# Kernel tuning notes

Measured on AMD Instinct MI355X. Metric: run time of the kernel, lower is better.

## Reference

```python
import jax, jax.numpy as jnp
from jax import lax
import numpy as np

B, H, W = 16, 512, 512
OPENING_R, EROSION_R, DILATION_R = 5, 2, 1
MIN_SIZE, AREA_THRESHOLD = 2000, 300
INF = np.int32(2 ** 30)


def _disk(r):
    # skimage.morphology.disk: x^2 + y^2 <= r^2 on a (2r+1)^2 grid
    y, x = np.mgrid[-r:r + 1, -r:r + 1]
    return jnp.asarray((x * x + y * y <= r * r).astype(np.float32))


D_OPEN, D_ERODE, D_DILATE = _disk(OPENING_R), _disk(EROSION_R), _disk(DILATION_R)


def _conv2(x, k):
    return lax.conv_general_dilated(x[None, None], k[None, None], (1, 1), 'VALID')[0, 0]


def _erode(fg, se):
    # skimage binary_erosion uses border_value=True (image border does not erode)
    r = se.shape[0] // 2
    x = jnp.pad(fg.astype(jnp.float32), r, constant_values=1.0)
    return _conv2(x, se) >= se.sum() - 0.5


def _dilate(fg, se):
    # skimage binary_dilation uses border_value=False
    r = se.shape[0] // 2
    x = jnp.pad(fg.astype(jnp.float32), r, constant_values=0.0)
    return _conv2(x, se) > 0.5


def _seg_cummin(v, reset, axis, reverse):
    # segmented cumulative-min: scan resets wherever `reset` is True (background)
    def comb(a, b):
        av, af = a
        bv, bf = b
        return jnp.where(bf, bv, jnp.minimum(av, bv)), af | bf

    vv, _ = lax.associative_scan(comb, (v, reset), axis=axis, reverse=reverse)
    return vv


def _label(fg):
    # 4-connectivity connected-component labeling via min-label propagation.
    # Each fg pixel starts with its raveled index; alternating row/col segmented
    # cummin sweeps run under while_loop until a fixed point (root id per comp).
    h, w = fg.shape
    idx = jnp.arange(h * w, dtype=jnp.int32).reshape(h, w)
    lab0 = jnp.where(fg, idx, INF)
    bg = ~fg

    def sweep(l):
        for axis in (1, 0):
            for rev in (False, True):
                l = jnp.where(fg, _seg_cummin(l, bg, axis, rev), INF)
        return l

    def body(c):
        l, _ = c
        nl = sweep(l)
        return nl, jnp.array_equal(nl, l)

    lab, _ = lax.while_loop(lambda c: ~c[1], body, (lab0, jnp.array(False)))
    seg = jnp.where(fg, lab, 0).ravel()
    sizes = jax.ops.segment_sum(fg.astype(jnp.int32).ravel(), seg, num_segments=h * w)
    ncomp = jnp.sum(sizes > 0)
    return lab, sizes, ncomp


def _remove_small_objects(fg, min_size, guard):
    lab, sizes, ncomp = _label(fg)
    px = sizes[jnp.where(fg, lab, 0)]  # component size at every fg pixel
    kept = fg & (px >= min_size)
    # original only removes small objects when label(...).max() > 1
    return jnp.where(ncomp > 1, kept, fg) if guard else kept


def _pipeline(mask):
    fg = mask > 0
    fg = _remove_small_objects(fg, MIN_SIZE, True)
    # remove_small_holes == ~remove_small_objects(~fg, area_threshold + 1)
    fg = ~_remove_small_objects(~fg, AREA_THRESHOLD + 1, False)
    fg = _erode(fg, D_ERODE)
    fg = _dilate(_erode(fg, D_OPEN), D_OPEN)  # binary_opening
    fg = _remove_small_objects(fg, MIN_SIZE, True)
    fg = _dilate(fg, D_DILATE)
    return fg.astype(jnp.float32)  # original casts to int; float32 kept for vjp parity


def setup_inputs() -> dict:
    key = jax.random.key(0)
    # blobby binary masks: threshold bilinearly-upsampled low-res noise so that
    # realistic large connected components (> min_size px) exist
    low = jax.random.uniform(key, (B, H // 16, W // 16), dtype=jnp.float32)
    blob = jax.image.resize(low, (B, H, W), method='bilinear')
    return {'inputs': (blob > 0.5).astype(jnp.float32)}


def reference(inputs):
    return jax.vmap(_pipeline)(inputs)
```

## Files before the change

kernel.cpp:

```cpp
#include <hip/hip_runtime.h>
#include <stdint.h>

#define BATCH 16
#define H 512
#define W 512
#define HW (H * W)
#define NTOT (BATCH * HW)
#define NWORDS (NTOT / 64)

#define TPB 256
#define NBLK ((NTOT + TPB - 1) / TPB)
#define NBLKW ((NWORDS + TPB - 1) / TPB)

#define SROWS 16
#define SWORDS 128
#define SPIX 8192
#define NSTRIPS (NWORDS / SWORDS)

__device__ __forceinline__ int find_root_c(int* L, int x) {
    int r = x, p = L[r];
    while (p != r) { r = p; p = L[r]; }
    if (L[x] != r) atomicMin(&L[x], r);
    return r;
}

__device__ void merge_uf(int* L, int a, int b) {
    while (true) {
        a = find_root_c(L, a);
        b = find_root_c(L, b);
        if (a == b) return;
        int lo = a < b ? a : b;
        int hi = a < b ? b : a;
        int old = atomicMin(&L[hi], lo);
        if (old == hi) return;
        a = lo; b = old;
    }
}

__device__ __forceinline__ int find_root_lds(int* P, int x) {
    int r = x, p = P[r];
    while (p != r) { r = p; p = P[r]; }
    return r;
}

__device__ void merge_lds(int* P, int a, int b) {
    while (true) {
        a = find_root_lds(P, a);
        b = find_root_lds(P, b);
        if (a == b) return;
        int lo = a < b ? a : b;
        int hi = a < b ? b : a;
        int old = atomicMin(&P[hi], lo);
        if (old == hi) return;
        a = lo; b = old;
    }
}

__device__ __forceinline__ int start_of(uint64_t m, int i, int cv, int base) {
    uint64_t below = i ? ((~m) & ((1ull << i) - 1)) : 0ull;
    if (below == 0) return (cv >= 0) ? cv : base;
    int hz = 63 - __builtin_clzll(below);
    return base + hz + 1;
}

__device__ uint64_t keep_word(const uint64_t* __restrict__ bits,
                              const int* __restrict__ carry, const int* __restrict__ L,
                              const int* __restrict__ sizes, const int* __restrict__ ncomp,
                              int minsz, int gw) {
    uint64_t m = bits[gw];
    uint64_t res = m;
    if (m && ncomp[gw >> 12] > 1) {
        int cv = carry[gw];
        int base = gw << 6;
        while (m) {
            int s = __builtin_ctzll(m);
            uint64_t rest = m >> s;
            uint64_t nr = ~rest;
            int len = nr ? __builtin_ctzll(nr) : (64 - s);
            uint64_t piece = ((len >= 64) ? ~0ull : ((1ull << len) - 1)) << s;
            int start = (s == 0 && cv >= 0) ? cv : (base + s);
            if (sizes[L[start]] < minsz) res &= ~piece;
            m &= ~piece;
        }
    }
    return res;
}

__device__ uint64_t fill_word(const uint64_t* __restrict__ bits,
                              const int* __restrict__ carry, const int* __restrict__ L,
                              const int* __restrict__ sizes, int minsz, int gw) {
    uint64_t fg = bits[gw];
    uint64_t bg = ~fg;
    uint64_t res = fg;
    int cv = carry[gw];
    int base = gw << 6;
    while (bg) {
        int s = __builtin_ctzll(bg);
        uint64_t rest = bg >> s;
        uint64_t nr = ~rest;
        int len = nr ? __builtin_ctzll(nr) : (64 - s);
        uint64_t piece = ((len >= 64) ? ~0ull : ((1ull << len) - 1)) << s;
        int start = (s == 0 && cv >= 0) ? cv : (base + s);
        if (sizes[L[start]] < minsz) res |= piece;
        bg &= ~piece;
    }
    return res;
}

template <int R, bool ERODE>
__device__ uint64_t morph_word_lds(const uint64_t* buf, int lrow, int w, int gyTop) {
    const uint64_t BORDER = ERODE ? ~0ull : 0ull;
    uint64_t res = ERODE ? ~0ull : 0ull;
#pragma unroll
    for (int dy = -R; dy <= R; ++dy) {
        int lr = lrow + dy;
        int gy = gyTop + lr;
        if (gy < 0 || gy >= H) continue;
        int v = R * R - dy * dy;
        int kx = 0;
        while ((kx + 1) * (kx + 1) <= v) ++kx;
        uint64_t cur = buf[lr * 8 + w];
        uint64_t prv = (w > 0) ? buf[lr * 8 + w - 1] : BORDER;
        uint64_t nxt = (w < 7) ? buf[lr * 8 + w + 1] : BORDER;
        uint64_t acc = cur;
#pragma unroll
        for (int dx = 1; dx <= kx; ++dx) {
            uint64_t right = (cur >> dx) | (nxt << (64 - dx));
            uint64_t left  = (cur << dx) | (prv >> (64 - dx));
            if (ERODE) acc &= right & left;
            else       acc |= right | left;
        }
        if (ERODE) res &= acc;
        else       res |= acc;
    }
    return res;
}

__device__ void strip_ccl_body(uint64_t m, uint64_t* sw, int* scarry, int* par,
                               int blk, int t,
                               int* __restrict__ carry, int* __restrict__ L,
                               int* __restrict__ sizes, int* __restrict__ ncomp) {
    sw[t] = m;
    __syncthreads();

    if (t < SROWS) {
        int cv = -1;
        for (int i = 0; i < 8; ++i) {
            int lw = t * 8 + i;
            scarry[lw] = cv;
            uint64_t w = sw[lw];
            if (w >> 63) {
                uint64_t z = ~w;
                if (z == 0) { if (cv < 0) cv = lw << 6; }
                else { int hz = 63 - __builtin_clzll(z); cv = (lw << 6) + hz + 1; }
            } else cv = -1;
        }
    }
    __syncthreads();

    int cv = scarry[t];
    carry[blk * SWORDS + t] = (cv >= 0) ? (blk * SPIX + cv) : -1;
    int lbase = t << 6;
    uint64_t starts = m & ~((m << 1) | ((cv >= 0) ? 1ull : 0ull));
    uint64_t ss = starts;
    while (ss) {
        int s = __builtin_ctzll(ss);
        par[lbase + s] = lbase + s;
        ss &= ss - 1;
    }
    __syncthreads();

    if (t >= 8 && m) {
        uint64_t up = sw[t - 8];
        uint64_t cand = m & up;
        if (cand) {
            uint64_t curprev = (t & 7) ? sw[t - 1] : 0ull;
            uint64_t upprev  = (t & 7) ? sw[t - 9] : 0ull;
            uint64_t curl = (m << 1) | (curprev >> 63);
            uint64_t upl  = (up << 1) | (upprev >> 63);
            cand &= ~(curl & upl);
            int cvu = scarry[t - 8];
            while (cand) {
                int i = __builtin_ctzll(cand);
                int sP = start_of(m, i, cv, lbase);
                int sQ = start_of(up, i, cvu, lbase - 512);
                merge_lds(par, sP, sQ);
                cand &= cand - 1;
            }
        }
    }
    __syncthreads();

    int gpix = blk * SPIX;
    ss = starts;
    while (ss) {
        int s = __builtin_ctzll(ss);
        int ls = lbase + s;
        int r = find_root_lds(par, ls);
        L[gpix + ls] = gpix + r;
        if (r == ls) sizes[gpix + ls] = 0;
        ss &= ss - 1;
    }
    if (t == 0 && (blk & 31) == 0) ncomp[blk >> 5] = 0;
}

__global__ void k_thresh_pack(const float* __restrict__ in, uint64_t* __restrict__ bits) {
    int p = blockIdx.x * blockDim.x + threadIdx.x;
    bool a = (p < NTOT) && (in[p] > 0.0f);
    uint64_t b = __ballot(a);
    if ((threadIdx.x & 63) == 0 && p < NTOT) bits[p >> 6] = b;
}

__global__ void k_strip_ccl(const uint64_t* __restrict__ bits, int inv,
                            int* __restrict__ carry, int* __restrict__ L,
                            int* __restrict__ sizes, int* __restrict__ ncomp) {
    __shared__ uint64_t sw[SWORDS];
    __shared__ int scarry[SWORDS];
    __shared__ int par[SPIX];
    int blk = blockIdx.x;
    int t = threadIdx.x;
    uint64_t inv64 = inv ? ~0ull : 0ull;
    uint64_t m = bits[blk * SWORDS + t] ^ inv64;
    strip_ccl_body(m, sw, scarry, par, blk, t, carry, L, sizes, ncomp);
}

__global__ void k_keep_strip(const uint64_t* __restrict__ bits,
                             const int* __restrict__ carryIn, const int* __restrict__ Lin,
                             const int* __restrict__ sizesIn, const int* __restrict__ ncompIn,
                             uint64_t* __restrict__ outBits,
                             int* __restrict__ carryOut, int* __restrict__ Lout,
                             int* __restrict__ sizesOut, int* __restrict__ ncompOut) {
    __shared__ uint64_t sw[SWORDS];
    __shared__ int scarry[SWORDS];
    __shared__ int par[SPIX];
    int blk = blockIdx.x;
    int t = threadIdx.x;
    int gw = blk * SWORDS + t;
    uint64_t kw = keep_word(bits, carryIn, Lin, sizesIn, ncompIn, 2000, gw);
    outBits[gw] = kw;
    strip_ccl_body(~kw, sw, scarry, par, blk, t, carryOut, Lout, sizesOut, ncompOut);
}

__global__ void k_merge_bound(const uint64_t* __restrict__ bits, int inv,
                              const int* __restrict__ carry, int* __restrict__ L) {
    int tid = threadIdx.x;
    if (tid >= 248) return;
    int img = blockIdx.x;
    int y = ((tid >> 3) + 1) * SROWS;
    int w = tid & 7;
    int gw = img * 4096 + y * 8 + w;
    uint64_t inv64 = inv ? ~0ull : 0ull;
    uint64_t cur = bits[gw] ^ inv64;
    uint64_t up  = bits[gw - 8] ^ inv64;
    uint64_t cand = cur & up;
    if (!cand) return;
    uint64_t curprev = w ? (bits[gw - 1] ^ inv64) : 0ull;
    uint64_t upprev  = w ? (bits[gw - 9] ^ inv64) : 0ull;
    uint64_t curl = (cur << 1) | (curprev >> 63);
    uint64_t upl  = (up << 1)  | (upprev >> 63);
    cand &= ~(curl & upl);
    if (!cand) return;
    int cvc = carry[gw], cvu = carry[gw - 8];
    int base = gw << 6;
    while (cand) {
        int i = __builtin_ctzll(cand);
        int sP = start_of(cur, i, cvc, base);
        int sQ = start_of(up, i, cvu, base - W);
        merge_uf(L, sP, sQ);
        cand &= cand - 1;
    }
}

__global__ void k_flatten_count(const uint64_t* __restrict__ bits, int inv,
                                const int* __restrict__ carry, int* __restrict__ L,
                                int* __restrict__ sizes, int* __restrict__ ncomp) {
    __shared__ int hk[128];
    __shared__ int hv[128];
    for (int i = threadIdx.x; i < 128; i += TPB) { hk[i] = -1; hv[i] = 0; }
    __syncthreads();

    int gw = blockIdx.x * blockDim.x + threadIdx.x;
    if (gw < NWORDS) {
        uint64_t inv64 = inv ? ~0ull : 0ull;
        uint64_t m = bits[gw] ^ inv64;
        if (m) {
            int cv = carry[gw];
            int base = gw << 6;
            while (m) {
                int s = __builtin_ctzll(m);
                uint64_t rest = m >> s;
                uint64_t nr = ~rest;
                int len = nr ? __builtin_ctzll(nr) : (64 - s);
                uint64_t piece = ((len >= 64) ? ~0ull : ((1ull << len) - 1)) << s;
                bool initial = !(s == 0 && cv >= 0);
                int start = initial ? (base + s) : cv;
                int r = find_root_c(L, start);
                if (initial && r == start) atomicAdd(&ncomp[gw >> 12], 1);
                int cnt = __popcll(piece);
                uint32_t h = ((uint32_t)r * 2654435761u) >> 25;
                bool done = false;
                for (int tt = 0; tt < 16; ++tt) {
                    int slot = (h + tt) & 127;
                    int k = hk[slot];
                    if (k == -1) k = atomicCAS(&hk[slot], -1, r);
                    if (k == -1 || k == r) { atomicAdd(&hv[slot], cnt); done = true; break; }
                }
                if (!done) atomicAdd(&sizes[r], cnt);
                m &= ~piece;
            }
        }
    }
    __syncthreads();
    for (int i = threadIdx.x; i < 128; i += TPB)
        if (hk[i] != -1) atomicAdd(&sizes[hk[i]], hv[i]);
}

__global__ void k_fill_morph(const uint64_t* __restrict__ bits,
                             const int* __restrict__ carry, const int* __restrict__ L,
                             const int* __restrict__ sizes,
                             uint64_t* __restrict__ out) {
    __shared__ uint64_t bufA[56 * 8];
    __shared__ uint64_t bufB[56 * 8];
    int img = blockIdx.x >> 4;
    int s   = blockIdx.x & 15;
    int y0 = s * 32;
    int gyTop = y0 - 12;
    int t = threadIdx.x;

    for (int lw = t; lw < 56 * 8; lw += TPB) {
        int gy = gyTop + (lw >> 3);
        int w = lw & 7;
        uint64_t v = 0;
        if (gy >= 0 && gy < H)
            v = fill_word(bits, carry, L, sizes, 301, img * 4096 + gy * 8 + w);
        bufA[lw] = v;
    }
    __syncthreads();

    for (int lw = t; lw < 56 * 8; lw += TPB) {
        int lr = lw >> 3;
        if (lr < 2 || lr > 53) continue;
        bufB[lw] = morph_word_lds<2, true>(bufA, lr, lw & 7, gyTop);
    }
    __syncthreads();

    for (int lw = t; lw < 56 * 8; lw += TPB) {
        int lr = lw >> 3;
        if (lr < 7 || lr > 48) continue;
        bufA[lw] = morph_word_lds<5, true>(bufB, lr, lw & 7, gyTop);
    }
    __syncthreads();

    for (int lw = t; lw < 56 * 8; lw += TPB) {
        int lr = lw >> 3;
        if (lr < 12 || lr > 43) continue;
        uint64_t v = morph_word_lds<5, false>(bufA, lr, lw & 7, gyTop);
        int gy = gyTop + lr;
        out[img * 4096 + gy * 8 + (lw & 7)] = v;
    }
}

__global__ void k_keep_dilate_float(const uint64_t* __restrict__ bits,
                                    const int* __restrict__ carry, const int* __restrict__ L,
                                    const int* __restrict__ sizes, const int* __restrict__ ncomp,
                                    float* __restrict__ out) {
    __shared__ uint64_t kb[10 * 8];
    __shared__ uint64_t db[8 * 8];
    int blk = blockIdx.x;
    int img = blk >> 6;
    int s = blk & 63;
    int y0 = s * 8;
    int t = threadIdx.x;

    if (t < 80) {
        int lr = t >> 3;
        int w = t & 7;
        int gy = y0 - 1 + lr;
        uint64_t v = 0;
        if (gy >= 0 && gy < H)
            v = keep_word(bits, carry, L, sizes, ncomp, 2000, img * 4096 + gy * 8 + w);
        kb[t] = v;
    }
    __syncthreads();
    if (t < 64) {
        int r = t >> 3, w = t & 7;
        uint64_t cur = kb[(r + 1) * 8 + w];
        uint64_t up  = kb[r * 8 + w];
        uint64_t dn  = kb[(r + 2) * 8 + w];
        uint64_t prv = w ? kb[(r + 1) * 8 + w - 1] : 0ull;
        uint64_t nxt = (w < 7) ? kb[(r + 1) * 8 + w + 1] : 0ull;
        db[t] = cur | up | dn | (cur << 1) | (prv >> 63) | (cur >> 1) | (nxt << 63);
    }
    __syncthreads();

    int q0 = t * 16;
    uint64_t wd = db[q0 >> 6];
    int sh = q0 & 63;
    float4* o = (float4*)(out + (size_t)img * HW + (size_t)y0 * W + q0);
#pragma unroll
    for (int k = 0; k < 4; ++k) {
        uint32_t nib = (uint32_t)(wd >> (sh + k * 4)) & 0xFu;
        float4 f;
        f.x = (nib & 1u) ? 1.0f : 0.0f;
        f.y = (nib & 2u) ? 1.0f : 0.0f;
        f.z = (nib & 4u) ? 1.0f : 0.0f;
        f.w = (nib & 8u) ? 1.0f : 0.0f;
        o[k] = f;
    }
}

extern "C" void kernel_launch(void* const* d_in, const int* in_sizes, int n_in,
                              void* d_out, int out_size, void* d_ws, size_t ws_size,
                              hipStream_t stream) {
    const float* in = (const float*)d_in[0];
    float* out = (float*)d_out;

    uint8_t* ws = (uint8_t*)d_ws;
    int* LA      = (int*)ws;
    int* sizesA  = (int*)(ws + (size_t)NTOT * 4);
    int* LB      = (int*)(ws + (size_t)NTOT * 8);
    int* sizesB  = (int*)(ws + (size_t)NTOT * 12);
    uint64_t* bitsA = (uint64_t*)(ws + (size_t)NTOT * 16);
    uint64_t* bitsB = bitsA + NWORDS;
    uint64_t* bits3 = bitsB + NWORDS;
    int* carryA = (int*)(bits3 + NWORDS);
    int* carryB = carryA + NWORDS;
    int* ncompA = carryB + NWORDS;
    int* ncompB = ncompA + BATCH;

    k_thresh_pack<<<NBLK, TPB, 0, stream>>>(in, bitsA);

    k_strip_ccl<<<NSTRIPS, SWORDS, 0, stream>>>(bitsA, 0, carryA, LA, sizesA, ncompA);
    k_merge_bound<<<BATCH, 256, 0, stream>>>(bitsA, 0, carryA, LA);
    k_flatten_count<<<NBLKW, TPB, 0, stream>>>(bitsA, 0, carryA, LA, sizesA, ncompA);

    k_keep_strip<<<NSTRIPS, SWORDS, 0, stream>>>(bitsA, carryA, LA, sizesA, ncompA,
                                                 bitsB, carryB, LB, sizesB, ncompB);
    k_merge_bound<<<BATCH, 256, 0, stream>>>(bitsB, 1, carryB, LB);
    k_flatten_count<<<NBLKW, TPB, 0, stream>>>(bitsB, 1, carryB, LB, sizesB, ncompB);

    k_fill_morph<<<BATCH * 16, TPB, 0, stream>>>(bitsB, carryB, LB, sizesB, bits3);

    k_strip_ccl<<<NSTRIPS, SWORDS, 0, stream>>>(bits3, 0, carryA, LA, sizesA, ncompA);
    k_merge_bound<<<BATCH, 256, 0, stream>>>(bits3, 0, carryA, LA);
    k_flatten_count<<<NBLKW, TPB, 0, stream>>>(bits3, 0, carryA, LA, sizesA, ncompA);

    k_keep_dilate_float<<<BATCH * 64, TPB, 0, stream>>>(bits3, carryA, LA, sizesA, ncompA, out);
}
```

Baseline: 204.0 us.

## Fuse CCL, fill and morphology stages into one cooperative persistent kernel

Replaces the sequence of nine launches (strip CCL, boundary merge, flatten/count for three labeling passes plus fill+morph) with a single cooperative kernel. Stages are separated by grid.sync, and the fill+morphology step is re-tiled to 16-row strips matching the CCL strip so it feeds the next labeling directly from LDS. The goal is to cut launch gaps and inter-kernel drain, at the cost of grid-wide barriers, 128-thread blocks and more redundant halo work in the morphology stage.

```diff
diff --git a/kernel.cpp b/kernel.cpp
--- a/kernel.cpp
+++ b/kernel.cpp
@@ -1,5 +1,8 @@
 #include <hip/hip_runtime.h>
+#include <hip/hip_cooperative_groups.h>
 #include <stdint.h>
+
+namespace cg = cooperative_groups;
 
 #define BATCH 16
 #define H 512
@@ -10,7 +13,6 @@
 
 #define TPB 256
 #define NBLK ((NTOT + TPB - 1) / TPB)
-#define NBLKW ((NWORDS + TPB - 1) / TPB)
 
 #define SROWS 16
 #define SWORDS 128
@@ -204,50 +206,14 @@
     if (t == 0 && (blk & 31) == 0) ncomp[blk >> 5] = 0;
 }
 
-__global__ void k_thresh_pack(const float* __restrict__ in, uint64_t* __restrict__ bits) {
-    int p = blockIdx.x * blockDim.x + threadIdx.x;
-    bool a = (p < NTOT) && (in[p] > 0.0f);
-    uint64_t b = __ballot(a);
-    if ((threadIdx.x & 63) == 0 && p < NTOT) bits[p >> 6] = b;
-}
-
-__global__ void k_strip_ccl(const uint64_t* __restrict__ bits, int inv,
-                            int* __restrict__ carry, int* __restrict__ L,
-                            int* __restrict__ sizes, int* __restrict__ ncomp) {
-    __shared__ uint64_t sw[SWORDS];
-    __shared__ int scarry[SWORDS];
-    __shared__ int par[SPIX];
-    int blk = blockIdx.x;
-    int t = threadIdx.x;
-    uint64_t inv64 = inv ? ~0ull : 0ull;
-    uint64_t m = bits[blk * SWORDS + t] ^ inv64;
-    strip_ccl_body(m, sw, scarry, par, blk, t, carry, L, sizes, ncomp);
-}
-
-__global__ void k_keep_strip(const uint64_t* __restrict__ bits,
-                             const int* __restrict__ carryIn, const int* __restrict__ Lin,
-                             const int* __restrict__ sizesIn, const int* __restrict__ ncompIn,
-                             uint64_t* __restrict__ outBits,
-                             int* __restrict__ carryOut, int* __restrict__ Lout,
-                             int* __restrict__ sizesOut, int* __restrict__ ncompOut) {
-    __shared__ uint64_t sw[SWORDS];
-    __shared__ int scarry[SWORDS];
-    __shared__ int par[SPIX];
-    int blk = blockIdx.x;
-    int t = threadIdx.x;
-    int gw = blk * SWORDS + t;
-    uint64_t kw = keep_word(bits, carryIn, Lin, sizesIn, ncompIn, 2000, gw);
-    outBits[gw] = kw;
-    strip_ccl_body(~kw, sw, scarry, par, blk, t, carryOut, Lout, sizesOut, ncompOut);
-}
-
-__global__ void k_merge_bound(const uint64_t* __restrict__ bits, int inv,
-                              const int* __restrict__ carry, int* __restrict__ L) {
-    int tid = threadIdx.x;
-    if (tid >= 248) return;
-    int img = blockIdx.x;
-    int y = ((tid >> 3) + 1) * SROWS;
-    int w = tid & 7;
+__device__ void merge_bound_dev(const uint64_t* __restrict__ bits, int inv,
+                                const int* __restrict__ carry, int* __restrict__ L,
+                                int flat) {
+    if (flat >= BATCH * 31 * 8) return;
+    int img = flat / 248;
+    int rem = flat - img * 248;
+    int y = ((rem >> 3) + 1) * SROWS;
+    int w = rem & 7;
     int gw = img * 4096 + y * 8 + w;
     uint64_t inv64 = inv ? ~0ull : 0ull;
     uint64_t cur = bits[gw] ^ inv64;
@@ -271,93 +237,125 @@
     }
 }
 
-__global__ void k_flatten_count(const uint64_t* __restrict__ bits, int inv,
-                                const int* __restrict__ carry, int* __restrict__ L,
-                                int* __restrict__ sizes, int* __restrict__ ncomp) {
+__device__ void flatten_count_dev(const uint64_t* __restrict__ bits, int inv,
+                                  const int* __restrict__ carry, int* __restrict__ L,
+                                  int* __restrict__ sizes, int* __restrict__ ncomp,
+                                  int gw, int t, int* hk, int* hv) {
+    hk[t] = -1; hv[t] = 0;
+    __syncthreads();
+    uint64_t inv64 = inv ? ~0ull : 0ull;
+    uint64_t m = bits[gw] ^ inv64;
+    if (m) {
+        int cv = carry[gw];
+        int base = gw << 6;
+        while (m) {
+            int s = __builtin_ctzll(m);
+            uint64_t rest = m >> s;
+            uint64_t nr = ~rest;
+            int len = nr ? __builtin_ctzll(nr) : (64 - s);
+            uint64_t piece = ((len >= 64) ? ~0ull : ((1ull << len) - 1)) << s;
+            bool initial = !(s == 0 && cv >= 0);
+            int start = initial ? (base + s) : cv;
+            int r = find_root_c(L, start);
+            if (initial && r == start) atomicAdd(&ncomp[gw >> 12], 1);
+            int cnt = __popcll(piece);
+            uint32_t h = ((uint32_t)r * 2654435761u) >> 25;
+            bool done = false;
+            for (int tt = 0; tt < 16; ++tt) {
+                int slot = (h + tt) & 127;
+                int k = hk[slot];
+                if (k == -1) k = atomicCAS(&hk[slot], -1, r);
+                if (k == -1 || k == r) { atomicAdd(&hv[slot], cnt); done = true; break; }
+            }
+            if (!done) atomicAdd(&sizes[r], cnt);
+            m &= ~piece;
+        }
+    }
+    __syncthreads();
+    if (hk[t] != -1) atomicAdd(&sizes[hk[t]], hv[t]);
+    __syncthreads();
+}
+
+__global__ void k_thresh_pack(const float* __restrict__ in, uint64_t* __restrict__ bits) {
+    int p = blockIdx.x * blockDim.x + threadIdx.x;
+    bool a = (p < NTOT) && (in[p] > 0.0f);
+    uint64_t b = __ballot(a);
+    if ((threadIdx.x & 63) == 0 && p < NTOT) bits[p >> 6] = b;
+}
+
+__global__ __launch_bounds__(SWORDS, 2)
+void k_mega(const uint64_t* __restrict__ bits1, uint64_t* __restrict__ bits2,
+            uint64_t* __restrict__ bits3,
+            int* __restrict__ carryA, int* __restrict__ carryB,
+            int* __restrict__ LA, int* __restrict__ LB,
+            int* __restrict__ sizesA, int* __restrict__ sizesB,
+            int* __restrict__ ncompA, int* __restrict__ ncompB) {
+    cg::grid_group grid = cg::this_grid();
+    __shared__ uint64_t sw[SWORDS];
+    __shared__ int scarry[SWORDS];
     __shared__ int hk[128];
     __shared__ int hv[128];
-    for (int i = threadIdx.x; i < 128; i += TPB) { hk[i] = -1; hv[i] = 0; }
-    __syncthreads();
-
-    int gw = blockIdx.x * blockDim.x + threadIdx.x;
-    if (gw < NWORDS) {
-        uint64_t inv64 = inv ? ~0ull : 0ull;
-        uint64_t m = bits[gw] ^ inv64;
-        if (m) {
-            int cv = carry[gw];
-            int base = gw << 6;
-            while (m) {
-                int s = __builtin_ctzll(m);
-                uint64_t rest = m >> s;
-                uint64_t nr = ~rest;
-                int len = nr ? __builtin_ctzll(nr) : (64 - s);
-                uint64_t piece = ((len >= 64) ? ~0ull : ((1ull << len) - 1)) << s;
-                bool initial = !(s == 0 && cv >= 0);
-                int start = initial ? (base + s) : cv;
-                int r = find_root_c(L, start);
-                if (initial && r == start) atomicAdd(&ncomp[gw >> 12], 1);
-                int cnt = __popcll(piece);
-                uint32_t h = ((uint32_t)r * 2654435761u) >> 25;
-                bool done = false;
-                for (int tt = 0; tt < 16; ++tt) {
-                    int slot = (h + tt) & 127;
-                    int k = hk[slot];
-                    if (k == -1) k = atomicCAS(&hk[slot], -1, r);
-                    if (k == -1 || k == r) { atomicAdd(&hv[slot], cnt); done = true; break; }
-                }
-                if (!done) atomicAdd(&sizes[r], cnt);
-                m &= ~piece;
-            }
-        }
-    }
-    __syncthreads();
-    for (int i = threadIdx.x; i < 128; i += TPB)
-        if (hk[i] != -1) atomicAdd(&sizes[hk[i]], hv[i]);
-}
-
-__global__ void k_fill_morph(const uint64_t* __restrict__ bits,
-                             const int* __restrict__ carry, const int* __restrict__ L,
-                             const int* __restrict__ sizes,
-                             uint64_t* __restrict__ out) {
-    __shared__ uint64_t bufA[56 * 8];
-    __shared__ uint64_t bufB[56 * 8];
-    int img = blockIdx.x >> 4;
-    int s   = blockIdx.x & 15;
-    int y0 = s * 32;
-    int gyTop = y0 - 12;
+    __shared__ union {
+        int par[SPIX];
+        struct { uint64_t A[320]; uint64_t B[320]; } mo;
+    } U;
+    int s = blockIdx.x;
     int t = threadIdx.x;
-
-    for (int lw = t; lw < 56 * 8; lw += TPB) {
-        int gy = gyTop + (lw >> 3);
-        int w = lw & 7;
-        uint64_t v = 0;
-        if (gy >= 0 && gy < H)
-            v = fill_word(bits, carry, L, sizes, 301, img * 4096 + gy * 8 + w);
-        bufA[lw] = v;
-    }
-    __syncthreads();
-
-    for (int lw = t; lw < 56 * 8; lw += TPB) {
-        int lr = lw >> 3;
-        if (lr < 2 || lr > 53) continue;
-        bufB[lw] = morph_word_lds<2, true>(bufA, lr, lw & 7, gyTop);
-    }
-    __syncthreads();
-
-    for (int lw = t; lw < 56 * 8; lw += TPB) {
-        int lr = lw >> 3;
-        if (lr < 7 || lr > 48) continue;
-        bufA[lw] = morph_word_lds<5, true>(bufB, lr, lw & 7, gyTop);
-    }
-    __syncthreads();
-
-    for (int lw = t; lw < 56 * 8; lw += TPB) {
-        int lr = lw >> 3;
-        if (lr < 12 || lr > 43) continue;
-        uint64_t v = morph_word_lds<5, false>(bufA, lr, lw & 7, gyTop);
-        int gy = gyTop + lr;
-        out[img * 4096 + gy * 8 + (lw & 7)] = v;
-    }
+    int gw = s * SWORDS + t;
+    int flat = s * SWORDS + t;
+
+    strip_ccl_body(bits1[gw], sw, scarry, U.par, s, t, carryA, LA, sizesA, ncompA);
+    grid.sync();
+    merge_bound_dev(bits1, 0, carryA, LA, flat);
+    grid.sync();
+    flatten_count_dev(bits1, 0, carryA, LA, sizesA, ncompA, gw, t, hk, hv);
+    grid.sync();
+
+    uint64_t kw = keep_word(bits1, carryA, LA, sizesA, ncompA, 2000, gw);
+    bits2[gw] = kw;
+    strip_ccl_body(~kw, sw, scarry, U.par, s, t, carryB, LB, sizesB, ncompB);
+    grid.sync();
+    merge_bound_dev(bits2, 1, carryB, LB, flat);
+    grid.sync();
+    flatten_count_dev(bits2, 1, carryB, LB, sizesB, ncompB, gw, t, hk, hv);
+    grid.sync();
+
+    uint64_t m3;
+    {
+        int img = s >> 5, si = s & 31;
+        int gyTop = si * 16 - 12;
+        for (int lw = t; lw < 320; lw += SWORDS) {
+            int gy = gyTop + (lw >> 3);
+            int w = lw & 7;
+            uint64_t v = 0;
+            if (gy >= 0 && gy < H)
+                v = fill_word(bits2, carryB, LB, sizesB, 301, img * 4096 + gy * 8 + w);
+            U.mo.A[lw] = v;
+        }
+        __syncthreads();
+        for (int lw = t; lw < 320; lw += SWORDS) {
+            int lr = lw >> 3;
+            if (lr >= 2 && lr <= 37) U.mo.B[lw] = morph_word_lds<2, true>(U.mo.A, lr, lw & 7, gyTop);
+        }
+        __syncthreads();
+        for (int lw = t; lw < 320; lw += SWORDS) {
+            int lr = lw >> 3;
+            if (lr >= 7 && lr <= 32) U.mo.A[lw] = morph_word_lds<5, true>(U.mo.B, lr, lw & 7, gyTop);
+        }
+        __syncthreads();
+        for (int lw = t; lw < 320; lw += SWORDS) {
+            int lr = lw >> 3;
+            if (lr >= 12 && lr <= 27) U.mo.B[lw] = morph_word_lds<5, false>(U.mo.A, lr, lw & 7, gyTop);
+        }
+        __syncthreads();
+        m3 = U.mo.B[t + 96];
+        bits3[gw] = m3;
+    }
+    strip_ccl_body(m3, sw, scarry, U.par, s, t, carryA, LA, sizesA, ncompA);
+    grid.sync();
+    merge_bound_dev(bits3, 0, carryA, LA, flat);
+    grid.sync();
+    flatten_count_dev(bits3, 0, carryA, LA, sizesA, ncompA, gw, t, hk, hv);
 }
 
 __global__ void k_keep_dilate_float(const uint64_t* __restrict__ bits,
@@ -420,30 +418,21 @@
     int* sizesA  = (int*)(ws + (size_t)NTOT * 4);
     int* LB      = (int*)(ws + (size_t)NTOT * 8);
     int* sizesB  = (int*)(ws + (size_t)NTOT * 12);
-    uint64_t* bitsA = (uint64_t*)(ws + (size_t)NTOT * 16);
-    uint64_t* bitsB = bitsA + NWORDS;
-    uint64_t* bits3 = bitsB + NWORDS;
+    uint64_t* bits1 = (uint64_t*)(ws + (size_t)NTOT * 16);
+    uint64_t* bits2 = bits1 + NWORDS;
+    uint64_t* bits3 = bits2 + NWORDS;
     int* carryA = (int*)(bits3 + NWORDS);
     int* carryB = carryA + NWORDS;
     int* ncompA = carryB + NWORDS;
     int* ncompB = ncompA + BATCH;
 
-    k_thresh_pack<<<NBLK, TPB, 0, stream>>>(in, bitsA);
-
-    k_strip_ccl<<<NSTRIPS, SWORDS, 0, stream>>>(bitsA, 0, carryA, LA, sizesA, ncompA);
-    k_merge_bound<<<BATCH, 256, 0, stream>>>(bitsA, 0, carryA, LA);
-    k_flatten_count<<<NBLKW, TPB, 0, stream>>>(bitsA, 0, carryA, LA, sizesA, ncompA);
-
-    k_keep_strip<<<NSTRIPS, SWORDS, 0, stream>>>(bitsA, carryA, LA, sizesA, ncompA,
-                                                 bitsB, carryB, LB, sizesB, ncompB);
-    k_merge_bound<<<BATCH, 256, 0, stream>>>(bitsB, 1, carryB, LB);
-    k_flatten_count<<<NBLKW, TPB, 0, stream>>>(bitsB, 1, carryB, LB, sizesB, ncompB);
-
-    k_fill_morph<<<BATCH * 16, TPB, 0, stream>>>(bitsB, carryB, LB, sizesB, bits3);
-
-    k_strip_ccl<<<NSTRIPS, SWORDS, 0, stream>>>(bits3, 0, carryA, LA, sizesA, ncompA);
-    k_merge_bound<<<BATCH, 256, 0, stream>>>(bits3, 0, carryA, LA);
-    k_flatten_count<<<NBLKW, TPB, 0, stream>>>(bits3, 0, carryA, LA, sizesA, ncompA);
+    k_thresh_pack<<<NBLK, TPB, 0, stream>>>(in, bits1);
+
+    void* args[] = { (void*)&bits1, (void*)&bits2, (void*)&bits3,
+                     (void*)&carryA, (void*)&carryB, (void*)&LA, (void*)&LB,
+                     (void*)&sizesA, (void*)&sizesB, (void*)&ncompA, (void*)&ncompB };
+    hipLaunchCooperativeKernel((void*)k_mega, dim3(NSTRIPS), dim3(SWORDS),
+                               args, 0, stream);
 
     k_keep_dilate_float<<<BATCH * 64, TPB, 0, stream>>>(bits3, carryA, LA, sizesA, ncompA, out);
 }
```

After: 621.3 us. 205% more time.

## Fuse hole-fill and morphology into strip CCL kernel; vectorize threshold packing

Applied to the files above, without the earlier changes.

Merges the fill+erode+open stage with the following per-strip connected-component labeling into one kernel. Each 16-row strip recomputes its morphology over a 12-row halo in LDS (a union with the CCL parent array) and then labels the result directly, which removes a launch and a global round trip of the intermediate mask. The cost is more halo recomputation per output row, since strips shrink from 32 rows to 16. The threshold-pack kernel also now reads float4 and combines nibbles with shuffles.

```diff
diff --git a/kernel.cpp b/kernel.cpp
--- a/kernel.cpp
+++ b/kernel.cpp
@@ -9,7 +9,6 @@
 #define NWORDS (NTOT / 64)
 
 #define TPB 256
-#define NBLK ((NTOT + TPB - 1) / TPB)
 #define NBLKW ((NWORDS + TPB - 1) / TPB)
 
 #define SROWS 16
@@ -204,11 +203,20 @@
     if (t == 0 && (blk & 31) == 0) ncomp[blk >> 5] = 0;
 }
 
-__global__ void k_thresh_pack(const float* __restrict__ in, uint64_t* __restrict__ bits) {
-    int p = blockIdx.x * blockDim.x + threadIdx.x;
-    bool a = (p < NTOT) && (in[p] > 0.0f);
-    uint64_t b = __ballot(a);
-    if ((threadIdx.x & 63) == 0 && p < NTOT) bits[p >> 6] = b;
+
+__global__ void k_thresh_pack4(const float4* __restrict__ in4,
+                               uint64_t* __restrict__ bits) {
+    int q = blockIdx.x * blockDim.x + threadIdx.x;
+    if (q >= NTOT / 4) return;
+    float4 v = in4[q];
+    uint32_t nib = (v.x > 0.0f ? 1u : 0u) | (v.y > 0.0f ? 2u : 0u) |
+                   (v.z > 0.0f ? 4u : 0u) | (v.w > 0.0f ? 8u : 0u);
+    uint64_t val = (uint64_t)nib << (4 * (threadIdx.x & 15));
+    val |= __shfl_xor(val, 1);
+    val |= __shfl_xor(val, 2);
+    val |= __shfl_xor(val, 4);
+    val |= __shfl_xor(val, 8);
+    if ((threadIdx.x & 15) == 0) bits[q >> 4] = val;
 }
 
 __global__ void k_strip_ccl(const uint64_t* __restrict__ bits, int inv,
@@ -315,49 +323,50 @@
         if (hk[i] != -1) atomicAdd(&sizes[hk[i]], hv[i]);
 }
 
-__global__ void k_fill_morph(const uint64_t* __restrict__ bits,
-                             const int* __restrict__ carry, const int* __restrict__ L,
-                             const int* __restrict__ sizes,
-                             uint64_t* __restrict__ out) {
-    __shared__ uint64_t bufA[56 * 8];
-    __shared__ uint64_t bufB[56 * 8];
-    int img = blockIdx.x >> 4;
-    int s   = blockIdx.x & 15;
-    int y0 = s * 32;
-    int gyTop = y0 - 12;
+__global__ void k_fill_morph_ccl(const uint64_t* __restrict__ bits,
+                                 const int* __restrict__ carryB, const int* __restrict__ LB,
+                                 const int* __restrict__ sizesB,
+                                 uint64_t* __restrict__ bits3,
+                                 int* __restrict__ carryA, int* __restrict__ LA,
+                                 int* __restrict__ sizesA, int* __restrict__ ncompA) {
+    __shared__ uint64_t sw[SWORDS];
+    __shared__ int scarry[SWORDS];
+    __shared__ union {
+        int par[SPIX];
+        struct { uint64_t A[320]; uint64_t B[320]; } mo;
+    } U;
+    int s = blockIdx.x;
     int t = threadIdx.x;
-
-    for (int lw = t; lw < 56 * 8; lw += TPB) {
+    int img = s >> 5, si = s & 31;
+    int gyTop = si * 16 - 12;
+
+    for (int lw = t; lw < 320; lw += SWORDS) {
         int gy = gyTop + (lw >> 3);
         int w = lw & 7;
         uint64_t v = 0;
         if (gy >= 0 && gy < H)
-            v = fill_word(bits, carry, L, sizes, 301, img * 4096 + gy * 8 + w);
-        bufA[lw] = v;
-    }
-    __syncthreads();
-
-    for (int lw = t; lw < 56 * 8; lw += TPB) {
+            v = fill_word(bits, carryB, LB, sizesB, 301, img * 4096 + gy * 8 + w);
+        U.mo.A[lw] = v;
+    }
+    __syncthreads();
+    for (int lw = t; lw < 320; lw += SWORDS) {
         int lr = lw >> 3;
-        if (lr < 2 || lr > 53) continue;
-        bufB[lw] = morph_word_lds<2, true>(bufA, lr, lw & 7, gyTop);
-    }
-    __syncthreads();
-
-    for (int lw = t; lw < 56 * 8; lw += TPB) {
+        if (lr >= 2 && lr <= 37) U.mo.B[lw] = morph_word_lds<2, true>(U.mo.A, lr, lw & 7, gyTop);
+    }
+    __syncthreads();
+    for (int lw = t; lw < 320; lw += SWORDS) {
         int lr = lw >> 3;
-        if (lr < 7 || lr > 48) continue;
-        bufA[lw] = morph_word_lds<5, true>(bufB, lr, lw & 7, gyTop);
-    }
-    __syncthreads();
-
-    for (int lw = t; lw < 56 * 8; lw += TPB) {
+        if (lr >= 7 && lr <= 32) U.mo.A[lw] = morph_word_lds<5, true>(U.mo.B, lr, lw & 7, gyTop);
+    }
+    __syncthreads();
+    for (int lw = t; lw < 320; lw += SWORDS) {
         int lr = lw >> 3;
-        if (lr < 12 || lr > 43) continue;
-        uint64_t v = morph_word_lds<5, false>(bufA, lr, lw & 7, gyTop);
-        int gy = gyTop + lr;
-        out[img * 4096 + gy * 8 + (lw & 7)] = v;
-    }
+        if (lr >= 12 && lr <= 27) U.mo.B[lw] = morph_word_lds<5, false>(U.mo.A, lr, lw & 7, gyTop);
+    }
+    __syncthreads();
+    uint64_t m3 = U.mo.B[t + 96];
+    bits3[s * SWORDS + t] = m3;
+    strip_ccl_body(m3, sw, scarry, U.par, s, t, carryA, LA, sizesA, ncompA);
 }
 
 __global__ void k_keep_dilate_float(const uint64_t* __restrict__ bits,
@@ -420,28 +429,27 @@
     int* sizesA  = (int*)(ws + (size_t)NTOT * 4);
     int* LB      = (int*)(ws + (size_t)NTOT * 8);
     int* sizesB  = (int*)(ws + (size_t)NTOT * 12);
-    uint64_t* bitsA = (uint64_t*)(ws + (size_t)NTOT * 16);
-    uint64_t* bitsB = bitsA + NWORDS;
-    uint64_t* bits3 = bitsB + NWORDS;
+    uint64_t* bits1 = (uint64_t*)(ws + (size_t)NTOT * 16);
+    uint64_t* bits2 = bits1 + NWORDS;
+    uint64_t* bits3 = bits2 + NWORDS;
     int* carryA = (int*)(bits3 + NWORDS);
     int* carryB = carryA + NWORDS;
     int* ncompA = carryB + NWORDS;
     int* ncompB = ncompA + BATCH;
 
-    k_thresh_pack<<<NBLK, TPB, 0, stream>>>(in, bitsA);
-
-    k_strip_ccl<<<NSTRIPS, SWORDS, 0, stream>>>(bitsA, 0, carryA, LA, sizesA, ncompA);
-    k_merge_bound<<<BATCH, 256, 0, stream>>>(bitsA, 0, carryA, LA);
-    k_flatten_count<<<NBLKW, TPB, 0, stream>>>(bitsA, 0, carryA, LA, sizesA, ncompA);
-
-    k_keep_strip<<<NSTRIPS, SWORDS, 0, stream>>>(bitsA, carryA, LA, sizesA, ncompA,
-                                                 bitsB, carryB, LB, sizesB, ncompB);
-    k_merge_bound<<<BATCH, 256, 0, stream>>>(bitsB, 1, carryB, LB);
-    k_flatten_count<<<NBLKW, TPB, 0, stream>>>(bitsB, 1, carryB, LB, sizesB, ncompB);
-
-    k_fill_morph<<<BATCH * 16, TPB, 0, stream>>>(bitsB, carryB, LB, sizesB, bits3);
-
-    k_strip_ccl<<<NSTRIPS, SWORDS, 0, stream>>>(bits3, 0, carryA, LA, sizesA, ncompA);
+    k_thresh_pack4<<<(NTOT / 4 + TPB - 1) / TPB, TPB, 0, stream>>>((const float4*)in, bits1);
+
+    k_strip_ccl<<<NSTRIPS, SWORDS, 0, stream>>>(bits1, 0, carryA, LA, sizesA, ncompA);
+    k_merge_bound<<<BATCH, 256, 0, stream>>>(bits1, 0, carryA, LA);
+    k_flatten_count<<<NBLKW, TPB, 0, stream>>>(bits1, 0, carryA, LA, sizesA, ncompA);
+
+    k_keep_strip<<<NSTRIPS, SWORDS, 0, stream>>>(bits1, carryA, LA, sizesA, ncompA,
+                                                 bits2, carryB, LB, sizesB, ncompB);
+    k_merge_bound<<<BATCH, 256, 0, stream>>>(bits2, 1, carryB, LB);
+    k_flatten_count<<<NBLKW, TPB, 0, stream>>>(bits2, 1, carryB, LB, sizesB, ncompB);
+
+    k_fill_morph_ccl<<<NSTRIPS, SWORDS, 0, stream>>>(bits2, carryB, LB, sizesB,
+                                                     bits3, carryA, LA, sizesA, ncompA);
     k_merge_bound<<<BATCH, 256, 0, stream>>>(bits3, 0, carryA, LA);
     k_flatten_count<<<NBLKW, TPB, 0, stream>>>(bits3, 0, carryA, LA, sizesA, ncompA);
 
```

Result: no change. 203.6 us (-0.2%).
